# Kernel tuning notes

Measured on AMD Instinct MI355X. Metric: run time of the kernel, lower is better.

Reference implementation:

```python
import jax, jax.numpy as jnp
import numpy as np

EPS = 1e-10
TOP_K = 2  # experts_per_token


def setup_inputs() -> dict:
    key = jax.random.key(0)
    k1, k2 = jax.random.split(key)
    dim, E = 2048, 64
    B, S = 4, 4096
    x = jax.random.normal(k1, (B * S, dim), dtype=jnp.float32)
    W = jax.random.normal(k2, (dim, E), dtype=jnp.float32) * (1.0 / np.sqrt(dim))
    b = jnp.zeros((E,), dtype=jnp.float32)
    return {"x": x, "W": W, "b": b, "batch_size": B, "seq_len": S}


def reference(x, W, b, batch_size, seq_len):
    E = W.shape[1]
    N = x.shape[0]  # batch_size * seq_len
    # gate + softmax + clamp
    scores = jax.nn.softmax(x @ W + b, axis=1)
    scores = jnp.clip(scores, EPS, 1.0 - EPS)
    # log-odds transform and rz loss over (seq, experts) per batch
    logits = jnp.log(scores / (1.0 - scores)).reshape(batch_size, seq_len, E)
    rz_loss = jnp.mean(jax.scipy.special.logsumexp(logits, axis=(1, 2)))
    # top-k experts per token
    top_scores, sel_idx = jax.lax.top_k(scores, TOP_K)  # (N, K) each
    flat_idx = sel_idx.reshape(-1)  # (N*K,)
    # histogram of assignments per expert (torch.histc with unit bins)
    num_tokens_per_expert = jax.ops.segment_sum(
        jnp.ones_like(flat_idx, dtype=jnp.float32), flat_idx, num_segments=E)
    # stable argsort groups slots by expert id, preserving token order
    perm = jnp.argsort(flat_idx, stable=True)  # (N*K,)
    top_scores_sorted = top_scores.reshape(-1)[perm]
    token_indices_experts_sorted = perm // TOP_K
    return (top_scores_sorted, token_indices_experts_sorted,
            num_tokens_per_expert, rz_loss)
```

## Files before the change

### kernel.cpp

```cpp
#include <hip/hip_runtime.h>
#include <math.h>

#define EPS_ 1e-10f
#define MARGIN 4e-3f

typedef __attribute__((ext_vector_type(8))) short sh8;
typedef __attribute__((ext_vector_type(4))) float fx4;

__device__ __forceinline__ bool betterf(float v, int i, float w, int j) {
    return (v > w) || (v == w && i < j);
}
__device__ __forceinline__ bool betterd(double v, int i, double w, int j) {
    return (v > w) || (v == w && i < j);
}
__device__ __forceinline__ unsigned short f2bf(float f) {
    unsigned u = __float_as_uint(f);
    u += 0x7fffu + ((u >> 16) & 1u);
    return (unsigned short)(u >> 16);
}
__device__ __forceinline__ float bf2f(unsigned short h) {
    return __uint_as_float(((unsigned)h) << 16);
}
__device__ __forceinline__ void cvt8(const float4 a, const float4 c, sh8& hi, sh8& lo) {
    const float v[8] = {a.x, a.y, a.z, a.w, c.x, c.y, c.z, c.w};
#pragma unroll
    for (int j = 0; j < 8; ++j) {
        const unsigned short h = f2bf(v[j]);
        hi[j] = (short)h;
        lo[j] = (short)f2bf(v[j] - bf2f(h));
    }
}
__device__ __forceinline__ void gload_lds16(const void* g, void* l) {
    __builtin_amdgcn_global_load_lds(
        (const __attribute__((address_space(1))) void*)g,
        (__attribute__((address_space(3))) void*)l, 16, 0, 0);
}

__global__ __launch_bounds__(256)
void wconv(const float* __restrict__ W, unsigned short* __restrict__ wf)
{
    const int gid = blockIdx.x * 256 + threadIdx.x;
    const int e = gid & 63, k = gid >> 6;
    const int s = k >> 5, kk = k & 31, bq = kk >> 3, j = kk & 7;
    const int t = e >> 4, n = e & 15;
    const int l = n + 16 * bq;
    const float w = W[(size_t)k * 64 + e];
    const unsigned short hi = f2bf(w);
    const unsigned short lo = f2bf(w - bf2f(hi));
    const size_t base = ((size_t)s * 4 + t) * 2;
    wf[(base + 0) * 512 + l * 8 + j] = hi;
    wf[(base + 1) * 512 + l * 8 + j] = lo;
}

#define KSPL 4
__global__ __launch_bounds__(256, 4)
void gemm_mfma(const float* __restrict__ x, const unsigned short* __restrict__ wfg,
               int dim, int N, float* __restrict__ zpart)
{
    __shared__ __align__(16) char xs[2][8192];
    __shared__ __align__(16) char wls[2][8192];

    const int tid  = threadIdx.x;
    const int lane = tid & 63;
    const int wv   = tid >> 6;
    const int rgs  = N / 64;
    const int ks   = blockIdx.x / rgs;
    const int rg   = blockIdx.x % rgs;
    const int r0   = rg * 64;
    const int kslice = dim / KSPL;
    const int k0   = ks * kslice;
    const int nstep = kslice / 32;

    const int m = lane & 15;
    const int q = lane >> 4;
    const int arow = wv * 16 + m;
    const int mk = m & 7;

    const int srow_in = lane >> 3;
    const int sgc     = (lane & 7) ^ (srow_in & 7);

    fx4 acc[4] = {};

    const char* wbytes = (const char*)wfg;
    const size_t wstep0 = (size_t)(k0 >> 5) * 8192;

#pragma unroll
    for (int r = 0; r < 2; ++r) {
        const int row = wv * 16 + r * 8 + srow_in;
        gload_lds16(x + (size_t)(r0 + row) * dim + k0 + sgc * 4,
                    &xs[0][(wv * 16 + r * 8) * 128]);
        gload_lds16(wbytes + wstep0 + wv * 2048 + r * 1024 + lane * 16,
                    &wls[0][wv * 2048 + r * 1024]);
    }
    __syncthreads();

    for (int s = 0; s < nstep; ++s) {
        const int cb = s & 1;
        if (s + 1 < nstep) {
#pragma unroll
            for (int r = 0; r < 2; ++r) {
                const int row = wv * 16 + r * 8 + srow_in;
                gload_lds16(x + (size_t)(r0 + row) * dim + k0 + (s + 1) * 32 + sgc * 4,
                            &xs[cb ^ 1][(wv * 16 + r * 8) * 128]);
                gload_lds16(wbytes + wstep0 + (size_t)(s + 1) * 8192
                                  + wv * 2048 + r * 1024 + lane * 16,
                            &wls[cb ^ 1][wv * 2048 + r * 1024]);
            }
        }
        {
            const float4 f0 = *(const float4*)&xs[cb][arow * 128 + ((2 * q + 0) ^ mk) * 16];
            const float4 f1 = *(const float4*)&xs[cb][arow * 128 + ((2 * q + 1) ^ mk) * 16];
            sh8 ah, al;
            cvt8(f0, f1, ah, al);
#pragma unroll
            for (int te = 0; te < 4; ++te) {
                const sh8 bh = __builtin_bit_cast(sh8,
                    *(const int4*)&wls[cb][(te * 2 + 0) * 1024 + lane * 16]);
                const sh8 bl = __builtin_bit_cast(sh8,
                    *(const int4*)&wls[cb][(te * 2 + 1) * 1024 + lane * 16]);
                acc[te] = __builtin_amdgcn_mfma_f32_16x16x32_bf16(ah, bh, acc[te], 0, 0, 0);
                acc[te] = __builtin_amdgcn_mfma_f32_16x16x32_bf16(ah, bl, acc[te], 0, 0, 0);
                acc[te] = __builtin_amdgcn_mfma_f32_16x16x32_bf16(al, bh, acc[te], 0, 0, 0);
            }
        }
        __syncthreads();
    }

    const int n = lane & 15;
    const int g = lane >> 4;
    float* zp = zpart + ((size_t)ks * N + r0 + wv * 16) * 64;
#pragma unroll
    for (int te = 0; te < 4; ++te)
#pragma unroll
        for (int i = 0; i < 4; ++i)
            zp[(g * 4 + i) * 64 + te * 16 + n] = acc[te][i];
}

__global__ __launch_bounds__(256)
void merge_epi(const float* __restrict__ zpart, const float* __restrict__ b,
               int N, float* __restrict__ ts, int* __restrict__ sel,
               float* __restrict__ rzrow,
               int* __restrict__ nflags, int* __restrict__ flaglist)
{
    const int lane = threadIdx.x & 63;
    const int wv   = threadIdx.x >> 6;
    const int e = lane;
    const float be = b[e];

    for (int rr = 0; rr < 4; ++rr) {
        const int row = blockIdx.x * 16 + wv * 4 + rr;
        float z = be;
#pragma unroll
        for (int ks = 0; ks < KSPL; ++ks)
            z += zpart[((size_t)ks * N + row) * 64 + e];

        float v1 = z, v2 = -3.4e38f;
        int i1 = e, i2 = 1 << 30;
#pragma unroll
        for (int mm = 1; mm < 64; mm <<= 1) {
            const float wva = __shfl_xor(v1, mm, 64); const int j1 = __shfl_xor(i1, mm, 64);
            const float wvb = __shfl_xor(v2, mm, 64); const int j2 = __shfl_xor(i2, mm, 64);
            if (betterf(wva, j1, v1, i1)) {
                float nv2; int ni2;
                if (betterf(v1, i1, wvb, j2)) { nv2 = v1; ni2 = i1; }
                else                          { nv2 = wvb; ni2 = j2; }
                v1 = wva; i1 = j1; v2 = nv2; i2 = ni2;
            } else if (betterf(wva, j1, v2, i2)) { v2 = wva; i2 = j1; }
        }

        float m3 = (e == i1 || e == i2) ? -3.4e38f : z;
#pragma unroll
        for (int mm = 1; mm < 64; mm <<= 1) m3 = fmaxf(m3, __shfl_xor(m3, mm, 64));

        const float ex = expf(z - v1);
        float ssum = ex;
#pragma unroll
        for (int mm = 1; mm < 64; mm <<= 1) ssum += __shfl_xor(ssum, mm, 64);
        const float inv = 1.0f / ssum;

        float sc = fminf(fmaxf(ex * inv, EPS_), 1.0f - EPS_);
        float srz = sc / (1.0f - sc);
#pragma unroll
        for (int mm = 1; mm < 64; mm <<= 1) srz += __shfl_xor(srz, mm, 64);

        if (e == 0) {
            const float s1 = fminf(fmaxf(inv, EPS_), 1.0f - EPS_);
            const float s2 = fminf(fmaxf(expf(v2 - v1) * inv, EPS_), 1.0f - EPS_);
            ts[row * 2 + 0] = s1;
            ts[row * 2 + 1] = s2;
            sel[row * 2 + 0] = i1;
            sel[row * 2 + 1] = i2;
            rzrow[row] = srz;
            if ((v1 - v2) < MARGIN || (v2 - m3) < MARGIN) {
                const int slot = atomicAdd(nflags, 1);
                flaglist[slot] = row;
            }
        }
    }
}

__global__ __launch_bounds__(1024)
void fixup(const float* __restrict__ x, const float* __restrict__ W,
           const float* __restrict__ b, int dim,
           const int* __restrict__ nflags, const int* __restrict__ flaglist,
           float* __restrict__ ts, int* __restrict__ sel)
{
    __shared__ double red[1024];
    const int tid = threadIdx.x;
    const int e = tid & 63;
    const int q = tid >> 6;
    const int nf = *nflags;
    const int slice = dim >> 4;

    for (int f = blockIdx.x; f < nf; f += gridDim.x) {
        const int row = flaglist[f];
        const float* xr = x + (size_t)row * dim;
        const int k0 = q * slice;
        double a0 = 0.0, a1 = 0.0, a2 = 0.0, a3 = 0.0;
        for (int k = k0; k < k0 + slice; k += 4) {
            a0 = fma((double)xr[k + 0], (double)W[(size_t)(k + 0) * 64 + e], a0);
            a1 = fma((double)xr[k + 1], (double)W[(size_t)(k + 1) * 64 + e], a1);
            a2 = fma((double)xr[k + 2], (double)W[(size_t)(k + 2) * 64 + e], a2);
            a3 = fma((double)xr[k + 3], (double)W[(size_t)(k + 3) * 64 + e], a3);
        }
        red[tid] = (a0 + a1) + (a2 + a3);
        __syncthreads();
        for (int st = 512; st >= 64; st >>= 1) {
            if (tid < st) red[tid] += red[tid + st];
            __syncthreads();
        }
        if (tid < 64) {
            const double z = red[tid] + (double)b[e];
            double v1 = z, v2 = -1e300;
            int i1 = e, i2 = 1 << 30;
#pragma unroll
            for (int mm = 1; mm < 64; mm <<= 1) {
                const double w1 = __shfl_xor(v1, mm, 64); const int j1 = __shfl_xor(i1, mm, 64);
                const double w2 = __shfl_xor(v2, mm, 64); const int j2 = __shfl_xor(i2, mm, 64);
                if (betterd(w1, j1, v1, i1)) {
                    double nv2; int ni2;
                    if (betterd(v1, i1, w2, j2)) { nv2 = v1; ni2 = i1; }
                    else                         { nv2 = w2; ni2 = j2; }
                    v1 = w1; i1 = j1; v2 = nv2; i2 = ni2;
                } else if (betterd(w1, j1, v2, i2)) { v2 = w1; i2 = j1; }
            }
            float sl = expf((float)(z - v1));
            float ssum = sl;
#pragma unroll
            for (int mm = 1; mm < 64; mm <<= 1) ssum += __shfl_xor(ssum, mm, 64);
            const float inv = 1.0f / ssum;
            if (e == 0) {
                const float s1 = fminf(fmaxf(inv, EPS_), 1.0f - EPS_);
                const float s2 = fminf(fmaxf(expf((float)(v2 - v1)) * inv, EPS_), 1.0f - EPS_);
                ts[row * 2 + 0] = s1;
                ts[row * 2 + 1] = s2;
                sel[row * 2 + 0] = i1;
                sel[row * 2 + 1] = i2;
            }
        }
        __syncthreads();
    }
}

__global__ void hist_chunks(const int* __restrict__ sel, int nchunks,
                            int* __restrict__ hist, int* __restrict__ cnt2)
{
    __shared__ int cnt[64];
    const int lane = threadIdx.x;
    const int c = blockIdx.x;
    cnt[lane] = 0;
    __syncthreads();
    const int ex = sel[c * 64 + lane];
    atomicAdd(&cnt[ex], 1);
    __syncthreads();
    cnt2[(size_t)lane * nchunks + c] = cnt[lane];
    if (cnt[lane]) atomicAdd(&hist[lane], cnt[lane]);
}

__global__ void rz_batch(const float* __restrict__ rzrow,
                         const int* __restrict__ bs_p, const int* __restrict__ sl_p,
                         double* __restrict__ bsum)
{
    __shared__ double red[256];
    const int nb = bs_p[0];
    const int seq = sl_p[0];
    for (int bb = blockIdx.x; bb < nb; bb += gridDim.x) {
        double s = 0.0;
        for (int i = threadIdx.x; i < seq; i += 256)
            s += (double)rzrow[(size_t)bb * seq + i];
        red[threadIdx.x] = s;
        __syncthreads();
        for (int st = 128; st > 0; st >>= 1) {
            if (threadIdx.x < st) red[threadIdx.x] += red[threadIdx.x + st];
            __syncthreads();
        }
        if (threadIdx.x == 0) bsum[bb] = red[0];
        __syncthreads();
    }
}

__global__ void combine(const int* __restrict__ hist,
                        int* __restrict__ estart,
                        const double* __restrict__ bsum,
                        const int* __restrict__ bs_p,
                        float* __restrict__ out_cnt, float* __restrict__ out_rz)
{
    const int e = threadIdx.x;
    const int c0 = hist[e];
    int incl = c0;
#pragma unroll
    for (int mm = 1; mm < 64; mm <<= 1) {
        const int w = __shfl_up(incl, mm, 64);
        if (e >= mm) incl += w;
    }
    estart[e] = incl - c0;
    out_cnt[e] = (float)c0;
    if (e == 0) {
        const int nb = bs_p[0];
        double a = 0.0;
        for (int i = 0; i < nb; ++i) a += log(bsum[i]);
        out_rz[0] = (float)(a / nb);
    }
}

__global__ __launch_bounds__(1024)
void chunk_scan(const int* __restrict__ cnt2, const int* __restrict__ estart,
                int nchunks, int* __restrict__ cbase)
{
    __shared__ int sc[1024];
    const int e = blockIdx.x;
    const int t = threadIdx.x;
    const int v = (t < nchunks) ? cnt2[(size_t)e * nchunks + t] : 0;
    sc[t] = v;
    __syncthreads();
#pragma unroll
    for (int off = 1; off < 1024; off <<= 1) {
        const int add = (t >= off) ? sc[t - off] : 0;
        __syncthreads();
        sc[t] += add;
        __syncthreads();
    }
    if (t < nchunks)
        cbase[(size_t)t * 64 + e] = estart[e] + sc[t] - v;
}

__global__ void scatter(const int* __restrict__ sel, const float* __restrict__ ts,
                        const int* __restrict__ cbase,
                        float* __restrict__ out_sc, float* __restrict__ out_idx)
{
    __shared__ int shx[64];
    const int lane = threadIdx.x;
    const int c = blockIdx.x;
    const int idx = c * 64 + lane;
    const int ex = sel[idx];
    shx[lane] = ex;
    __syncthreads();
    int pre = 0;
#pragma unroll
    for (int j = 0; j < 64; ++j) pre += (int)((j < lane) && (shx[j] == ex));
    const int pos = cbase[c * 64 + ex] + pre;
    out_sc[pos]  = ts[idx];
    out_idx[pos] = (float)(idx >> 1);
}

extern "C" void kernel_launch(void* const* d_in, const int* in_sizes, int n_in,
                              void* d_out, int out_size, void* d_ws, size_t ws_size,
                              hipStream_t stream)
{
    const float* x = (const float*)d_in[0];
    const float* W = (const float*)d_in[1];
    const float* b = (const float*)d_in[2];
    const int* bs_p = (const int*)d_in[3];
    const int* sl_p = (const int*)d_in[4];

    const int E   = in_sizes[2];
    const int dim = in_sizes[1] / E;
    const int N   = in_sizes[0] / dim;
    const int total = N * 2;
    const int nchunks = total / 64;

    char* ws = (char*)d_ws;
    size_t off = 0;
    int*    hist     = (int*)(ws + off); off += 256;
    double* bsum     = (double*)(ws + off); off += 512;
    int*    nflags   = (int*)(ws + off); off += 256;
    int*    estart   = (int*)(ws + off); off += 256;
    float*  ts       = (float*)(ws + off); off += (size_t)total * 4;
    int*    sel      = (int*)(ws + off); off += (size_t)total * 4;
    int*    flaglist = (int*)(ws + off); off += (size_t)N * 4;
    float*  rzrow    = (float*)(ws + off); off += (size_t)N * 4;
    int*    cnt2     = (int*)(ws + off); off += (size_t)nchunks * 64 * 4;
    int*    cbase    = (int*)(ws + off); off += (size_t)nchunks * 64 * 4;
    unsigned short* wfg = (unsigned short*)(ws + off); off += (size_t)dim * 64 * 2 * 2;
    float*  zpart    = (float*)(ws + off); off += (size_t)KSPL * N * 64 * 4;

    float* out_sc  = (float*)d_out;
    float* out_idx = out_sc + total;
    float* out_cnt = out_idx + total;
    float* out_rz  = out_cnt + E;

    hipMemsetAsync(ws, 0, 1280, stream);

    hipLaunchKernelGGL(wconv, dim3(dim * 64 / 256), dim3(256), 0, stream, W, wfg);
    hipLaunchKernelGGL(gemm_mfma, dim3((N / 64) * KSPL), dim3(256), 0, stream,
                       x, wfg, dim, N, zpart);
    hipLaunchKernelGGL(merge_epi, dim3(N / 16), dim3(256), 0, stream,
                       zpart, b, N, ts, sel, rzrow, nflags, flaglist);
    hipLaunchKernelGGL(fixup, dim3(512), dim3(1024), 0, stream,
                       x, W, b, dim, nflags, flaglist, ts, sel);
    hipLaunchKernelGGL(hist_chunks, dim3(nchunks), dim3(64), 0, stream,
                       sel, nchunks, hist, cnt2);
    hipLaunchKernelGGL(rz_batch, dim3(64), dim3(256), 0, stream,
                       rzrow, bs_p, sl_p, bsum);
    hipLaunchKernelGGL(combine, dim3(1), dim3(64), 0, stream,
                       hist, estart, bsum, bs_p, out_cnt, out_rz);
    hipLaunchKernelGGL(chunk_scan, dim3(64), dim3(1024), 0, stream,
                       cnt2, estart, nchunks, cbase);
    hipLaunchKernelGGL(scatter, dim3(nchunks), dim3(64), 0, stream,
                       sel, ts, cbase, out_sc, out_idx);
}
```

Before: 95.25 us.

## Fuse histogram and rz reduction into merge epilogue, merge combine into scan

The merge epilogue now processes 32 rows per block, matching the 64-slot chunk size. It builds the per-chunk expert histogram in shared memory and accumulates the per-batch rz sum with a double atomic. The fixup kernel patches the histogram and chunk counts when it changes a row's selection. The combine kernel is folded into the chunk scan via a serial prefix in thread 0. Together these remove three kernel launches and the rzrow round trip, at the cost of global atomics and fewer merge blocks.

```diff
diff --git a/kernel.cpp b/kernel.cpp
--- a/kernel.cpp
+++ b/kernel.cpp
@@ -137,18 +137,30 @@
 }
 
 __global__ __launch_bounds__(256)
-void merge_epi(const float* __restrict__ zpart, const float* __restrict__ b,
-               int N, float* __restrict__ ts, int* __restrict__ sel,
-               float* __restrict__ rzrow,
-               int* __restrict__ nflags, int* __restrict__ flaglist)
-{
-    const int lane = threadIdx.x & 63;
-    const int wv   = threadIdx.x >> 6;
-    const int e = lane;
+void merge_epi32(const float* __restrict__ zpart, const float* __restrict__ b,
+                 const int* __restrict__ sl_p, int N, int nchunks,
+                 float* __restrict__ ts, int* __restrict__ sel,
+                 int* __restrict__ nflags, int* __restrict__ flaglist,
+                 int* __restrict__ hist, int* __restrict__ cnt2,
+                 double* __restrict__ bsum)
+{
+    __shared__ int cnt[64];
+    __shared__ float rsum[4];
+
+    const int tid  = threadIdx.x;
+    const int lane = tid & 63;
+    const int wv   = tid >> 6;
+    const int c    = blockIdx.x;
+    const int e    = lane;
     const float be = b[e];
 
-    for (int rr = 0; rr < 4; ++rr) {
-        const int row = blockIdx.x * 16 + wv * 4 + rr;
+    if (tid < 64) cnt[tid] = 0;
+    __syncthreads();
+
+    float myrz = 0.0f;
+
+    for (int rr = 0; rr < 8; ++rr) {
+        const int row = c * 32 + wv * 8 + rr;
         float z = be;
 #pragma unroll
         for (int ks = 0; ks < KSPL; ++ks)
@@ -190,20 +202,36 @@
             ts[row * 2 + 1] = s2;
             sel[row * 2 + 0] = i1;
             sel[row * 2 + 1] = i2;
-            rzrow[row] = srz;
+            atomicAdd(&cnt[i1], 1);
+            atomicAdd(&cnt[i2], 1);
+            myrz += srz;
             if ((v1 - v2) < MARGIN || (v2 - m3) < MARGIN) {
                 const int slot = atomicAdd(nflags, 1);
                 flaglist[slot] = row;
             }
         }
     }
+
+    if (lane == 0) rsum[wv] = myrz;
+    __syncthreads();
+
+    if (tid < 64) {
+        cnt2[(size_t)tid * nchunks + c] = cnt[tid];
+        if (cnt[tid]) atomicAdd(&hist[tid], cnt[tid]);
+    }
+    if (tid == 0) {
+        const int seq = sl_p[0];
+        const int batch = (c * 32) / seq;
+        atomicAdd(&bsum[batch], (double)(rsum[0] + rsum[1] + rsum[2] + rsum[3]));
+    }
 }
 
 __global__ __launch_bounds__(1024)
 void fixup(const float* __restrict__ x, const float* __restrict__ W,
-           const float* __restrict__ b, int dim,
+           const float* __restrict__ b, int dim, int nchunks,
            const int* __restrict__ nflags, const int* __restrict__ flaglist,
-           float* __restrict__ ts, int* __restrict__ sel)
+           float* __restrict__ ts, int* __restrict__ sel,
+           int* __restrict__ hist, int* __restrict__ cnt2)
 {
     __shared__ double red[1024];
     const int tid = threadIdx.x;
@@ -252,84 +280,50 @@
             if (e == 0) {
                 const float s1 = fminf(fmaxf(inv, EPS_), 1.0f - EPS_);
                 const float s2 = fminf(fmaxf(expf((float)(v2 - v1)) * inv, EPS_), 1.0f - EPS_);
+                const int o1 = sel[row * 2 + 0];
+                const int o2 = sel[row * 2 + 1];
                 ts[row * 2 + 0] = s1;
                 ts[row * 2 + 1] = s2;
-                sel[row * 2 + 0] = i1;
-                sel[row * 2 + 1] = i2;
+                if (o1 != i1 || o2 != i2) {
+                    sel[row * 2 + 0] = i1;
+                    sel[row * 2 + 1] = i2;
+                    const int c = row >> 5;
+                    atomicSub(&hist[o1], 1); atomicSub(&hist[o2], 1);
+                    atomicAdd(&hist[i1], 1); atomicAdd(&hist[i2], 1);
+                    atomicSub(&cnt2[(size_t)o1 * nchunks + c], 1);
+                    atomicSub(&cnt2[(size_t)o2 * nchunks + c], 1);
+                    atomicAdd(&cnt2[(size_t)i1 * nchunks + c], 1);
+                    atomicAdd(&cnt2[(size_t)i2 * nchunks + c], 1);
+                }
             }
         }
         __syncthreads();
     }
 }
 
-__global__ void hist_chunks(const int* __restrict__ sel, int nchunks,
-                            int* __restrict__ hist, int* __restrict__ cnt2)
-{
-    __shared__ int cnt[64];
-    const int lane = threadIdx.x;
-    const int c = blockIdx.x;
-    cnt[lane] = 0;
-    __syncthreads();
-    const int ex = sel[c * 64 + lane];
-    atomicAdd(&cnt[ex], 1);
-    __syncthreads();
-    cnt2[(size_t)lane * nchunks + c] = cnt[lane];
-    if (cnt[lane]) atomicAdd(&hist[lane], cnt[lane]);
-}
-
-__global__ void rz_batch(const float* __restrict__ rzrow,
-                         const int* __restrict__ bs_p, const int* __restrict__ sl_p,
-                         double* __restrict__ bsum)
-{
-    __shared__ double red[256];
-    const int nb = bs_p[0];
-    const int seq = sl_p[0];
-    for (int bb = blockIdx.x; bb < nb; bb += gridDim.x) {
-        double s = 0.0;
-        for (int i = threadIdx.x; i < seq; i += 256)
-            s += (double)rzrow[(size_t)bb * seq + i];
-        red[threadIdx.x] = s;
-        __syncthreads();
-        for (int st = 128; st > 0; st >>= 1) {
-            if (threadIdx.x < st) red[threadIdx.x] += red[threadIdx.x + st];
-            __syncthreads();
-        }
-        if (threadIdx.x == 0) bsum[bb] = red[0];
-        __syncthreads();
-    }
-}
-
-__global__ void combine(const int* __restrict__ hist,
-                        int* __restrict__ estart,
-                        const double* __restrict__ bsum,
-                        const int* __restrict__ bs_p,
-                        float* __restrict__ out_cnt, float* __restrict__ out_rz)
-{
-    const int e = threadIdx.x;
-    const int c0 = hist[e];
-    int incl = c0;
-#pragma unroll
-    for (int mm = 1; mm < 64; mm <<= 1) {
-        const int w = __shfl_up(incl, mm, 64);
-        if (e >= mm) incl += w;
-    }
-    estart[e] = incl - c0;
-    out_cnt[e] = (float)c0;
-    if (e == 0) {
-        const int nb = bs_p[0];
-        double a = 0.0;
-        for (int i = 0; i < nb; ++i) a += log(bsum[i]);
-        out_rz[0] = (float)(a / nb);
-    }
-}
-
 __global__ __launch_bounds__(1024)
-void chunk_scan(const int* __restrict__ cnt2, const int* __restrict__ estart,
-                int nchunks, int* __restrict__ cbase)
+void scan2(const int* __restrict__ hist, const int* __restrict__ cnt2,
+           int nchunks, int* __restrict__ cbase,
+           const double* __restrict__ bsum, const int* __restrict__ bs_p,
+           float* __restrict__ out_cnt, float* __restrict__ out_rz)
 {
     __shared__ int sc[1024];
+    __shared__ int es;
     const int e = blockIdx.x;
     const int t = threadIdx.x;
+
+    if (t == 0) {
+        int s = 0;
+        for (int i = 0; i < e; ++i) s += hist[i];
+        es = s;
+        out_cnt[e] = (float)hist[e];
+        if (e == 0) {
+            const int nb = bs_p[0];
+            double a = 0.0;
+            for (int i = 0; i < nb; ++i) a += log(bsum[i]);
+            out_rz[0] = (float)(a / nb);
+        }
+    }
     const int v = (t < nchunks) ? cnt2[(size_t)e * nchunks + t] : 0;
     sc[t] = v;
     __syncthreads();
@@ -341,7 +335,7 @@
         __syncthreads();
     }
     if (t < nchunks)
-        cbase[(size_t)t * 64 + e] = estart[e] + sc[t] - v;
+        cbase[(size_t)t * 64 + e] = es + sc[t] - v;
 }
 
 __global__ void scatter(const int* __restrict__ sel, const float* __restrict__ ts,
@@ -384,11 +378,9 @@
     int*    hist     = (int*)(ws + off); off += 256;
     double* bsum     = (double*)(ws + off); off += 512;
     int*    nflags   = (int*)(ws + off); off += 256;
-    int*    estart   = (int*)(ws + off); off += 256;
     float*  ts       = (float*)(ws + off); off += (size_t)total * 4;
     int*    sel      = (int*)(ws + off); off += (size_t)total * 4;
     int*    flaglist = (int*)(ws + off); off += (size_t)N * 4;
-    float*  rzrow    = (float*)(ws + off); off += (size_t)N * 4;
     int*    cnt2     = (int*)(ws + off); off += (size_t)nchunks * 64 * 4;
     int*    cbase    = (int*)(ws + off); off += (size_t)nchunks * 64 * 4;
     unsigned short* wfg = (unsigned short*)(ws + off); off += (size_t)dim * 64 * 2 * 2;
@@ -399,23 +391,18 @@
     float* out_cnt = out_idx + total;
     float* out_rz  = out_cnt + E;
 
-    hipMemsetAsync(ws, 0, 1280, stream);
+    hipMemsetAsync(ws, 0, 1024, stream);
 
     hipLaunchKernelGGL(wconv, dim3(dim * 64 / 256), dim3(256), 0, stream, W, wfg);
     hipLaunchKernelGGL(gemm_mfma, dim3((N / 64) * KSPL), dim3(256), 0, stream,
                        x, wfg, dim, N, zpart);
-    hipLaunchKernelGGL(merge_epi, dim3(N / 16), dim3(256), 0, stream,
-                       zpart, b, N, ts, sel, rzrow, nflags, flaglist);
+    hipLaunchKernelGGL(merge_epi32, dim3(nchunks), dim3(256), 0, stream,
+                       zpart, b, sl_p, N, nchunks, ts, sel, nflags, flaglist,
+                       hist, cnt2, bsum);
     hipLaunchKernelGGL(fixup, dim3(512), dim3(1024), 0, stream,
-                       x, W, b, dim, nflags, flaglist, ts, sel);
-    hipLaunchKernelGGL(hist_chunks, dim3(nchunks), dim3(64), 0, stream,
-                       sel, nchunks, hist, cnt2);
-    hipLaunchKernelGGL(rz_batch, dim3(64), dim3(256), 0, stream,
-                       rzrow, bs_p, sl_p, bsum);
-    hipLaunchKernelGGL(combine, dim3(1), dim3(64), 0, stream,
-                       hist, estart, bsum, bs_p, out_cnt, out_rz);
-    hipLaunchKernelGGL(chunk_scan, dim3(64), dim3(1024), 0, stream,
-                       cnt2, estart, nchunks, cbase);
+                       x, W, b, dim, nchunks, nflags, flaglist, ts, sel, hist, cnt2);
+    hipLaunchKernelGGL(scan2, dim3(64), dim3(1024), 0, stream,
+                       hist, cnt2, nchunks, cbase, bsum, bs_p, out_cnt, out_rz);
     hipLaunchKernelGGL(scatter, dim3(nchunks), dim3(64), 0, stream,
                        sel, ts, cbase, out_sc, out_idx);
 }
```

Result: faster. 90.78 us (median of 2 runs) (-4.7%).
